# Performance work log

Hardware: AMD Instinct MI355X
Metric: run time of the kernel (lower is better)

The kernel has to match this reference:

```python
import jax, jax.numpy as jnp
import numpy as np
from jax import lax

# Dimensions (ModelArgs with d_model=1024)
B, L = 2, 1024
D_MODEL = 1024
D_INNER = 2048          # expand * d_model
D_STATE = 16
DT_RANK = 64            # ceil(d_model / 16)
D_CONV = 4


def setup_inputs() -> dict:
    key = jax.random.key(0)
    ks = jax.random.split(key, 8)
    sc = lambda k, shp, s: jax.random.normal(k, shp, dtype=jnp.float32) * s
    x = jax.random.normal(ks[0], (B, L, D_MODEL), dtype=jnp.float32)
    W_in = sc(ks[1], (2 * D_INNER, D_MODEL), 0.02)
    conv_w = sc(ks[2], (D_INNER, D_CONV), 0.2)
    conv_b = jnp.zeros((D_INNER,), jnp.float32)
    W_x = sc(ks[3], (DT_RANK + 2 * D_STATE, D_INNER), 0.02)
    dt_init_std = DT_RANK ** -0.5
    W_dt = jax.random.uniform(ks[4], (D_INNER, DT_RANK), jnp.float32,
                              -dt_init_std, dt_init_std)
    # dt_proj bias: inverse-softplus of dt ~ logUniform(dt_min, dt_max)
    dt_min, dt_max = 1e-3, 1e-1
    u = jax.random.uniform(ks[5], (D_INNER,), jnp.float32)
    dt = jnp.exp(u * (np.log(dt_max) - np.log(dt_min)) + np.log(dt_min))
    dt = jnp.clip(dt, 1e-4, None)
    b_dt = dt + jnp.log(-jnp.expm1(-dt))
    A_log = jnp.log(jnp.tile(jnp.arange(1, D_STATE + 1, dtype=jnp.float32)[None, :],
                             (D_INNER, 1)))
    D = jnp.ones((D_INNER,), jnp.float32)
    W_out = sc(ks[6], (D_MODEL, D_INNER), 0.02)
    return {"x": x, "W_in": W_in, "conv_w": conv_w, "conv_b": conv_b,
            "W_x": W_x, "W_dt": W_dt, "b_dt": b_dt, "A_log": A_log,
            "D": D, "W_out": W_out}


def reference(x, W_in, conv_w, conv_b, W_x, W_dt, b_dt, A_log, D, W_out):
    b, l, _ = x.shape
    d_in, n = A_log.shape
    k = conv_w.shape[1]

    # in_proj, split into conv branch and gating residual
    x_and_res = x @ W_in.T                                 # (b, l, 2*d_in)
    xz, res = jnp.split(x_and_res, [d_in], axis=-1)

    # Causal depthwise conv1d (kernel k, left-pad k-1, truncate to l)
    xp = jnp.pad(xz, ((0, 0), (k - 1, 0), (0, 0)))         # (b, l+k-1, d_in)
    xc = conv_b[None, None, :] + sum(
        xp[:, i:i + l, :] * conv_w[None, None, :, i] for i in range(k))
    xc = jax.nn.silu(xc)                                   # (b, l, d_in)

    # x_proj -> delta, B, C
    x_dbl = xc @ W_x.T                                     # (b, l, dt_rank+2n)
    dlt, Bm, Cm = jnp.split(x_dbl, [DT_RANK, DT_RANK + n], axis=-1)
    delta = jax.nn.softplus(dlt @ W_dt.T + b_dt)           # (b, l, d_in)

    # selective scan
    A = -jnp.exp(A_log)                                    # (d_in, n)
    dA = jnp.exp(delta[..., None] * A[None, None])         # (b, l, d_in, n)
    dBu = (delta * xc)[..., None] * Bm[:, :, None, :]      # (b, l, d_in, n)

    def step(h, inp):
        dA_t, dBu_t, C_t = inp                             # (b,d,n),(b,d,n),(b,n)
        h = dA_t * h + dBu_t
        y = jnp.einsum('bdn,bn->bd', h, C_t)
        return h, y

    h0 = jnp.zeros((b, d_in, n), xc.dtype)
    _, ys = lax.scan(step, h0, (dA.transpose(1, 0, 2, 3),
                                dBu.transpose(1, 0, 2, 3),
                                Cm.transpose(1, 0, 2)))
    y = ys.transpose(1, 0, 2) + xc * D[None, None, :]      # (b, l, d_in)

    y = y * jax.nn.silu(res)
    return y @ W_out.T                                     # (b, l, d_model)
```

## Files before the change

kernel.cpp:

```cpp
#include <hip/hip_runtime.h>
#include <hip/hip_bf16.h>
#include <cmath>

#define DEV __device__ __forceinline__

typedef float  f32x4  __attribute__((ext_vector_type(4)));
typedef __bf16 bf16x8 __attribute__((ext_vector_type(8)));
using u16 = unsigned short;

constexpr int CB   = 2;
constexpr int CLEN = 1024;
constexpr int CDM  = 1024;
constexpr int CDI  = 2048;
constexpr int CM   = CB * CLEN;
constexpr int NCHUNK = 32;
constexpr int CHL    = 32;
constexpr int LS     = 40;

DEV u16 f2bf(float f) {
  unsigned u = __builtin_bit_cast(unsigned, f);
  unsigned r = (u + 0x7fffu + ((u >> 16) & 1u)) >> 16;
  return (u16)r;
}
DEV float bf2f(u16 v) { return __builtin_bit_cast(float, ((unsigned)v) << 16); }

DEV ushort4 f4bf(float4 v) {
  ushort4 o;
  o.x = f2bf(v.x); o.y = f2bf(v.y); o.z = f2bf(v.z); o.w = f2bf(v.w);
  return o;
}

constexpr int CG_X   = 524288;
constexpr int CG_WIN = CG_X   + 1048576;
constexpr int CG_WDT = CG_WIN + 32768;
constexpr int CG_WO  = CG_WDT + 524288;
constexpr int CG_WX  = CG_WO  + 65536;

__global__ void cast_all_k(const float* __restrict__ x, const float* __restrict__ W_in,
                           const float* __restrict__ W_dt, const float* __restrict__ W_out,
                           const float* __restrict__ W_x,
                           u16* __restrict__ xb, u16* __restrict__ W_inb,
                           u16* __restrict__ W_dtb, u16* __restrict__ W_outb,
                           u16* __restrict__ W_xb)
{
  int i = blockIdx.x * blockDim.x + threadIdx.x;
  if (i < CG_X) {
    reinterpret_cast<ushort4*>(xb)[i] = f4bf(reinterpret_cast<const float4*>(x)[i]);
  } else if (i < CG_WIN) {
    int j = i - CG_X;
    reinterpret_cast<ushort4*>(W_inb)[j] = f4bf(reinterpret_cast<const float4*>(W_in)[j]);
  } else if (i < CG_WDT) {
    int j = i - CG_WIN;
    reinterpret_cast<ushort4*>(W_dtb)[j] = f4bf(reinterpret_cast<const float4*>(W_dt)[j]);
  } else if (i < CG_WO) {
    int j = i - CG_WDT;
    reinterpret_cast<ushort4*>(W_outb)[j] = f4bf(reinterpret_cast<const float4*>(W_out)[j]);
  } else {
    int j = i - CG_WO;
    int base = j * 4, row = base >> 11, col = base & 2047;
    float4 v = make_float4(0.f, 0.f, 0.f, 0.f);
    if (row < 96) v = *reinterpret_cast<const float4*>(W_x + row * 2048 + col);
    reinterpret_cast<ushort4*>(W_xb)[j] = f4bf(v);
  }
}

template <int EPI, int SPLITK>
__global__ __launch_bounds__(256, 2)
void gemm_bt(const u16* __restrict__ A, const u16* __restrict__ Bw,
             float* __restrict__ C, u16* __restrict__ Cb,
             const float* __restrict__ bias,
             int Nd, int Kd, int lda, int ldb, int ldc, size_t slice_stride)
{
  __shared__ u16 As[128 * LS];
  __shared__ u16 Bs[128 * LS];
  const int tid  = threadIdx.x;
  const int wave = tid >> 6;
  const int lane = tid & 63;
  const int wm = wave >> 1, wn = wave & 1;
  const int row0 = blockIdx.y * 128;
  const int col0 = blockIdx.x * 128;
  const int lr = lane >> 2;
  const int lc = (lane & 3) * 8;

  const int kper = Kd / SPLITK;
  const int kbeg = (SPLITK > 1) ? blockIdx.z * kper : 0;
  const int kend = kbeg + kper;
  float* Cz = (SPLITK > 1) ? C + (size_t)blockIdx.z * slice_stride : C;

  const u16* Ag = A  + (size_t)(row0 + wave * 16 + lr) * lda + lc;
  const u16* Bg = Bw + (size_t)(col0 + wave * 16 + lr) * ldb + lc;
  u16* Al0 = As + (wave * 16 + lr) * LS + lc;
  u16* Al1 = As + (64 + wave * 16 + lr) * LS + lc;
  u16* Bl0 = Bs + (wave * 16 + lr) * LS + lc;
  u16* Bl1 = Bs + (64 + wave * 16 + lr) * LS + lc;

  bf16x8 pa0 = *reinterpret_cast<const bf16x8*>(Ag + kbeg);
  bf16x8 pa1 = *reinterpret_cast<const bf16x8*>(Ag + (size_t)64 * lda + kbeg);
  bf16x8 pb0 = *reinterpret_cast<const bf16x8*>(Bg + kbeg);
  bf16x8 pb1 = *reinterpret_cast<const bf16x8*>(Bg + (size_t)64 * ldb + kbeg);

  f32x4 acc[4][4] = {};
  const int q  = lane >> 4;
  const int mr = lane & 15;

  for (int k0 = kbeg; k0 < kend; k0 += 32) {
    __syncthreads();
    *reinterpret_cast<bf16x8*>(Al0) = pa0;
    *reinterpret_cast<bf16x8*>(Al1) = pa1;
    *reinterpret_cast<bf16x8*>(Bl0) = pb0;
    *reinterpret_cast<bf16x8*>(Bl1) = pb1;
    __syncthreads();
    const int k1 = (k0 + 32 < kend) ? k0 + 32 : kbeg;
    pa0 = *reinterpret_cast<const bf16x8*>(Ag + k1);
    pa1 = *reinterpret_cast<const bf16x8*>(Ag + (size_t)64 * lda + k1);
    pb0 = *reinterpret_cast<const bf16x8*>(Bg + k1);
    pb1 = *reinterpret_cast<const bf16x8*>(Bg + (size_t)64 * ldb + k1);

    bf16x8 af[4], bfr[4];
#pragma unroll
    for (int t = 0; t < 4; ++t) {
      af[t]  = *reinterpret_cast<const bf16x8*>(As + (wm * 64 + t * 16 + mr) * LS + q * 8);
      bfr[t] = *reinterpret_cast<const bf16x8*>(Bs + (wn * 64 + t * 16 + mr) * LS + q * 8);
    }
#pragma unroll
    for (int mt = 0; mt < 4; ++mt)
#pragma unroll
      for (int nt = 0; nt < 4; ++nt)
        acc[mt][nt] = __builtin_amdgcn_mfma_f32_16x16x32_bf16(af[mt], bfr[nt], acc[mt][nt], 0, 0, 0);
  }

  const int cn = lane & 15;
#pragma unroll
  for (int mt = 0; mt < 4; ++mt)
#pragma unroll
    for (int nt = 0; nt < 4; ++nt)
#pragma unroll
      for (int r = 0; r < 4; ++r) {
        const int row = row0 + wm * 64 + mt * 16 + q * 4 + r;
        const int col = col0 + wn * 64 + nt * 16 + cn;
        float v = acc[mt][nt][r];
        if (EPI == 3) {
          v += bias[col];
          v = (v > 15.f) ? v : log1pf(__expf(v));
        }
        if (EPI == 0) Cz[(size_t)row * ldc + col] = v;
        else          Cb[(size_t)row * ldc + col] = f2bf(v);
      }
}

__global__ void xdbl_reduce_k(const float* __restrict__ part,
                              float* __restrict__ xdbl, u16* __restrict__ xdblb)
{
  int i = blockIdx.x * blockDim.x + threadIdx.x;
  float4 s = reinterpret_cast<const float4*>(part)[i];
#pragma unroll
  for (int z = 1; z < 16; ++z) {
    float4 p = reinterpret_cast<const float4*>(part + (size_t)z * CM * 128)[i];
    s.x += p.x; s.y += p.y; s.z += p.z; s.w += p.w;
  }
  reinterpret_cast<float4*>(xdbl)[i] = s;
  reinterpret_cast<ushort4*>(xdblb)[i] = f4bf(s);
}

__global__ void out_reduce_k(const float* __restrict__ part, float* __restrict__ out)
{
  int i = blockIdx.x * blockDim.x + threadIdx.x;
  float4 s = reinterpret_cast<const float4*>(part)[i];
#pragma unroll
  for (int z = 1; z < 4; ++z) {
    float4 p = reinterpret_cast<const float4*>(part + (size_t)z * CM * CDM)[i];
    s.x += p.x; s.y += p.y; s.z += p.z; s.w += p.w;
  }
  reinterpret_cast<float4*>(out)[i] = s;
}

__global__ void conv_silu_k(const u16* __restrict__ xzb, const float4* __restrict__ cw4,
                            const float* __restrict__ cb, u16* __restrict__ xcb)
{
  int idx = blockIdx.x * blockDim.x + threadIdx.x;
  int d8  = (idx & (CDI / 8 - 1)) * 8;
  int row = idx >> 8;
  int l   = row & (CLEN - 1);

  float4 wv[8];
#pragma unroll
  for (int j = 0; j < 8; ++j) wv[j] = cw4[d8 + j];
  float acc[8];
#pragma unroll
  for (int j = 0; j < 8; ++j) acc[j] = cb[d8 + j];

#pragma unroll
  for (int i = 0; i < 4; ++i) {
    int ls = l - 3 + i;
    if (ls >= 0) {
      bf16x8 v = *reinterpret_cast<const bf16x8*>(xzb + (size_t)(row - l + ls) * 4096 + d8);
#pragma unroll
      for (int j = 0; j < 8; ++j) {
        const float* wp = (const float*)&wv[j];
        acc[j] += (float)v[j] * wp[i];
      }
    }
  }
  bf16x8 o;
#pragma unroll
  for (int j = 0; j < 8; ++j) {
    float s = acc[j] / (1.f + __expf(-acc[j]));
    o[j] = (__bf16)s;
  }
  *reinterpret_cast<bf16x8*>(xcb + (size_t)row * CDI + d8) = o;
}

__global__ __launch_bounds__(256)
void scan_p1(const u16* __restrict__ delta_b, const u16* __restrict__ xcb,
             const float* __restrict__ xdbl, const float* __restrict__ A_log,
             float* __restrict__ P, float* __restrict__ S)
{
  __shared__ float sB[CHL * 16];
  const int t = threadIdx.x;
  const int d = blockIdx.x * 256 + t;
  const int c = blockIdx.y, b = blockIdx.z;

  for (int i = t; i < CHL * 16; i += 256) {
    int ll = i >> 4, n = i & 15;
    sB[i] = xdbl[(size_t)(b * CLEN + c * CHL + ll) * 128 + 64 + n];
  }
  __syncthreads();

  float An[16], Pv[16], Sv[16];
#pragma unroll
  for (int n = 0; n < 16; ++n) {
    An[n] = -__expf(A_log[d * 16 + n]);
    Pv[n] = 1.f; Sv[n] = 0.f;
  }
  const size_t rbase = (size_t)(b * CLEN + c * CHL) * CDI + d;
  for (int ll = 0; ll < CHL; ++ll) {
    float dl = bf2f(delta_b[rbase + (size_t)ll * CDI]);
    float u  = bf2f(xcb[rbase + (size_t)ll * CDI]);
    float du = dl * u;
#pragma unroll
    for (int n = 0; n < 16; ++n) {
      float a = __expf(dl * An[n]);
      Pv[n] *= a;
      Sv[n] = a * Sv[n] + du * sB[ll * 16 + n];
    }
  }
  const size_t o = (size_t)((b * NCHUNK + c) * 16) * CDI + d;
#pragma unroll
  for (int n = 0; n < 16; ++n) {
    P[o + (size_t)n * CDI] = Pv[n];
    S[o + (size_t)n * CDI] = Sv[n];
  }
}

__global__ void scan_p2(const float* __restrict__ P, const float* __restrict__ S,
                        float* __restrict__ Hin)
{
  const int t = threadIdx.x;
  const int d = blockIdx.x * 256 + t;
  const int n = blockIdx.y, b = blockIdx.z;
  float h = 0.f;
#pragma unroll 8
  for (int c = 0; c < NCHUNK; ++c) {
    size_t o = (size_t)((b * NCHUNK + c) * 16 + n) * CDI + d;
    Hin[o] = h;
    h = P[o] * h + S[o];
  }
}

__global__ __launch_bounds__(256)
void scan_p3(const u16* __restrict__ delta_b, const u16* __restrict__ xcb,
             const float* __restrict__ xdbl, const float* __restrict__ A_log,
             const float* __restrict__ Dvec, const u16* __restrict__ xzb,
             const float* __restrict__ Hin, u16* __restrict__ ybarb)
{
  __shared__ float sB[CHL * 16];
  __shared__ float sC[CHL * 16];
  const int t = threadIdx.x;
  const int d = blockIdx.x * 256 + t;
  const int c = blockIdx.y, b = blockIdx.z;

  for (int i = t; i < CHL * 16; i += 256) {
    int ll = i >> 4, n = i & 15;
    size_t ro = (size_t)(b * CLEN + c * CHL + ll) * 128;
    sB[i] = xdbl[ro + 64 + n];
    sC[i] = xdbl[ro + 80 + n];
  }
  __syncthreads();

  float An[16], h[16];
  const size_t ho = (size_t)((b * NCHUNK + c) * 16) * CDI + d;
#pragma unroll
  for (int n = 0; n < 16; ++n) {
    An[n] = -__expf(A_log[d * 16 + n]);
    h[n]  = Hin[ho + (size_t)n * CDI];
  }
  const float Dd = Dvec[d];
  const size_t rbase = (size_t)(b * CLEN + c * CHL);
  for (int ll = 0; ll < CHL; ++ll) {
    size_t e = (rbase + ll) * CDI + d;
    float dl = bf2f(delta_b[e]);
    float u  = bf2f(xcb[e]);
    float du = dl * u;
    float y  = 0.f;
#pragma unroll
    for (int n = 0; n < 16; ++n) {
      float a = __expf(dl * An[n]);
      h[n] = a * h[n] + du * sB[ll * 16 + n];
      y += h[n] * sC[ll * 16 + n];
    }
    y += u * Dd;
    float r = bf2f(xzb[(rbase + ll) * 4096 + CDI + d]);
    float sr = r / (1.f + __expf(-r));
    ybarb[e] = f2bf(y * sr);
  }
}

extern "C" void kernel_launch(void* const* d_in, const int* in_sizes, int n_in,
                              void* d_out, int out_size, void* d_ws, size_t ws_size,
                              hipStream_t stream)
{
  (void)in_sizes; (void)n_in; (void)out_size; (void)ws_size;
  const float* x      = (const float*)d_in[0];
  const float* W_in   = (const float*)d_in[1];
  const float* conv_w = (const float*)d_in[2];
  const float* conv_b = (const float*)d_in[3];
  const float* W_x    = (const float*)d_in[4];
  const float* W_dt   = (const float*)d_in[5];
  const float* b_dt   = (const float*)d_in[6];
  const float* A_log  = (const float*)d_in[7];
  const float* Dvec   = (const float*)d_in[8];
  const float* W_out  = (const float*)d_in[9];
  float* out = (float*)d_out;

  constexpr size_t MB = 1048576;
  char* w = (char*)d_ws;
  u16*   xzres_b = (u16*)(w + 0);
  u16*   xb      = (u16*)(w + 16 * MB);
  u16*   W_inb   = (u16*)(w + 20 * MB);
  u16*   xcb     = (u16*)(w + 28 * MB);
  u16*   delta_b = (u16*)(w + 36 * MB);
  float* xpart   = (float*)(w + 44 * MB);
  float* xdbl    = (float*)(w + 60 * MB);
  u16*   xdblb   = (u16*)(w + 61 * MB);
  u16*   W_xb    = (u16*)(w + 61 * MB + 512 * 1024);
  u16*   W_dtb   = (u16*)(w + 62 * MB);
  float* Pb      = (float*)(w + 63 * MB);
  float* Sb      = (float*)(w + 71 * MB);
  float* Hin     = (float*)(w + 79 * MB);
  u16*   ybarb   = (u16*)(w + 87 * MB);
  u16*   W_outb  = (u16*)(w + 95 * MB);
  float* opart   = (float*)(w + 99 * MB);

  dim3 blk(256);
  cast_all_k<<<CG_WX / 256, blk, 0, stream>>>(x, W_in, W_dt, W_out, W_x,
                                              xb, W_inb, W_dtb, W_outb, W_xb);
  gemm_bt<1, 1><<<dim3(32, 16), blk, 0, stream>>>(xb, W_inb, nullptr, xzres_b, nullptr,
                                                  4096, 1024, 1024, 1024, 4096, 0);
  conv_silu_k<<<(CB * CLEN * CDI / 8) / 256, blk, 0, stream>>>(
      xzres_b, (const float4*)conv_w, conv_b, xcb);
  gemm_bt<0, 16><<<dim3(1, 16, 16), blk, 0, stream>>>(xcb, W_xb, xpart, nullptr, nullptr,
                                                      128, 2048, 2048, 2048, 128,
                                                      (size_t)CM * 128);
  xdbl_reduce_k<<<(CM * 128 / 4) / 256, blk, 0, stream>>>(xpart, xdbl, xdblb);
  gemm_bt<3, 1><<<dim3(16, 16), blk, 0, stream>>>(xdblb, W_dtb, nullptr, delta_b, b_dt,
                                                  2048, 64, 128, 64, 2048, 0);
  scan_p1<<<dim3(8, NCHUNK, 2), blk, 0, stream>>>(delta_b, xcb, xdbl, A_log, Pb, Sb);
  scan_p2<<<dim3(8, 16, 2), blk, 0, stream>>>(Pb, Sb, Hin);
  scan_p3<<<dim3(8, NCHUNK, 2), blk, 0, stream>>>(delta_b, xcb, xdbl, A_log, Dvec,
                                                  xzres_b, Hin, ybarb);
  gemm_bt<0, 4><<<dim3(8, 16, 4), blk, 0, stream>>>(ybarb, W_outb, opart, nullptr, nullptr,
                                                    1024, 2048, 2048, 2048, 1024,
                                                    (size_t)CM * CDM);
  out_reduce_k<<<(CM * CDM / 4) / 256, blk, 0, stream>>>(opart, out);
}
```

Before: 259.1 us.

## Fuse three-pass chunked scan into single decoupled-lookback kernel

Replaces the three scan kernels (chunk-local pass, sequential carry pass, recompute-and-output pass) with one kernel. It uses atomic ticket ordering and per-chunk flags with decoupled lookback to pass inclusive states between chunks. Delta and x values are kept in registers between the local pass and the output pass, so they are not reloaded from global memory. This removes two launches and the separate P/S/Hin round trip. In exchange it adds spin-waiting on flags and serial dependence across chunk blocks, and register pressure rises from the 32-entry buffer.

Result: slower. 724.8 us (+179.8%).

```diff
diff --git a/kernel.cpp b/kernel.cpp
--- a/kernel.cpp
+++ b/kernel.cpp
@@ -41,9 +41,10 @@
                            const float* __restrict__ W_x,
                            u16* __restrict__ xb, u16* __restrict__ W_inb,
                            u16* __restrict__ W_dtb, u16* __restrict__ W_outb,
-                           u16* __restrict__ W_xb)
+                           u16* __restrict__ W_xb, int* __restrict__ flags)
 {
   int i = blockIdx.x * blockDim.x + threadIdx.x;
+  if (i < 1024) flags[i] = 0;
   if (i < CG_X) {
     reinterpret_cast<ushort4*>(xb)[i] = f4bf(reinterpret_cast<const float4*>(x)[i]);
   } else if (i < CG_WIN) {
@@ -210,74 +211,27 @@
   *reinterpret_cast<bf16x8*>(xcb + (size_t)row * CDI + d8) = o;
 }
 
-__global__ __launch_bounds__(256)
-void scan_p1(const u16* __restrict__ delta_b, const u16* __restrict__ xcb,
-             const float* __restrict__ xdbl, const float* __restrict__ A_log,
-             float* __restrict__ P, float* __restrict__ S)
-{
-  __shared__ float sB[CHL * 16];
-  const int t = threadIdx.x;
-  const int d = blockIdx.x * 256 + t;
-  const int c = blockIdx.y, b = blockIdx.z;
-
-  for (int i = t; i < CHL * 16; i += 256) {
-    int ll = i >> 4, n = i & 15;
-    sB[i] = xdbl[(size_t)(b * CLEN + c * CHL + ll) * 128 + 64 + n];
-  }
-  __syncthreads();
-
-  float An[16], Pv[16], Sv[16];
-#pragma unroll
-  for (int n = 0; n < 16; ++n) {
-    An[n] = -__expf(A_log[d * 16 + n]);
-    Pv[n] = 1.f; Sv[n] = 0.f;
-  }
-  const size_t rbase = (size_t)(b * CLEN + c * CHL) * CDI + d;
-  for (int ll = 0; ll < CHL; ++ll) {
-    float dl = bf2f(delta_b[rbase + (size_t)ll * CDI]);
-    float u  = bf2f(xcb[rbase + (size_t)ll * CDI]);
-    float du = dl * u;
-#pragma unroll
-    for (int n = 0; n < 16; ++n) {
-      float a = __expf(dl * An[n]);
-      Pv[n] *= a;
-      Sv[n] = a * Sv[n] + du * sB[ll * 16 + n];
-    }
-  }
-  const size_t o = (size_t)((b * NCHUNK + c) * 16) * CDI + d;
-#pragma unroll
-  for (int n = 0; n < 16; ++n) {
-    P[o + (size_t)n * CDI] = Pv[n];
-    S[o + (size_t)n * CDI] = Sv[n];
-  }
-}
-
-__global__ void scan_p2(const float* __restrict__ P, const float* __restrict__ S,
-                        float* __restrict__ Hin)
-{
-  const int t = threadIdx.x;
-  const int d = blockIdx.x * 256 + t;
-  const int n = blockIdx.y, b = blockIdx.z;
-  float h = 0.f;
-#pragma unroll 8
-  for (int c = 0; c < NCHUNK; ++c) {
-    size_t o = (size_t)((b * NCHUNK + c) * 16 + n) * CDI + d;
-    Hin[o] = h;
-    h = P[o] * h + S[o];
-  }
-}
-
-__global__ __launch_bounds__(256)
-void scan_p3(const u16* __restrict__ delta_b, const u16* __restrict__ xcb,
-             const float* __restrict__ xdbl, const float* __restrict__ A_log,
-             const float* __restrict__ Dvec, const u16* __restrict__ xzb,
-             const float* __restrict__ Hin, u16* __restrict__ ybarb)
+__global__ __launch_bounds__(256, 2)
+void scan_fused(const u16* __restrict__ delta_b, const u16* __restrict__ xcb,
+                const float* __restrict__ xdbl, const float* __restrict__ A_log,
+                const float* __restrict__ Dvec, const u16* __restrict__ xzb,
+                float* __restrict__ Ploc, float* __restrict__ Sloc,
+                float* __restrict__ Sinc, int* __restrict__ flags,
+                u16* __restrict__ ybarb)
 {
   __shared__ float sB[CHL * 16];
   __shared__ float sC[CHL * 16];
+  __shared__ int s_ticket;
   const int t = threadIdx.x;
-  const int d = blockIdx.x * 256 + t;
-  const int c = blockIdx.y, b = blockIdx.z;
+  if (t == 0) s_ticket = atomicAdd(&flags[512], 1);
+  __syncthreads();
+  const int ticket = s_ticket;
+  const int c    = ticket >> 4;
+  const int idx  = ticket & 15;
+  const int dblk = idx & 7;
+  const int b    = idx >> 3;
+  const int d    = dblk * 256 + t;
+  const int lane = t & 63;
 
   for (int i = t; i < CHL * 16; i += 256) {
     int ll = i >> 4, n = i & 15;
@@ -287,19 +241,96 @@
   }
   __syncthreads();
 
-  float An[16], h[16];
-  const size_t ho = (size_t)((b * NCHUNK + c) * 16) * CDI + d;
+  float An[16], Pv[16], Sv[16];
 #pragma unroll
   for (int n = 0; n < 16; ++n) {
     An[n] = -__expf(A_log[d * 16 + n]);
-    h[n]  = Hin[ho + (size_t)n * CDI];
-  }
+    Pv[n] = 1.f; Sv[n] = 0.f;
+  }
+
+  unsigned dx[CHL];
+  const size_t rbase = (size_t)(b * CLEN + c * CHL) * CDI + d;
+  for (int ll = 0; ll < CHL; ++ll) {
+    u16 dl16 = delta_b[rbase + (size_t)ll * CDI];
+    u16 uc16 = xcb[rbase + (size_t)ll * CDI];
+    dx[ll] = (unsigned)dl16 | ((unsigned)uc16 << 16);
+    float dl = bf2f(dl16), u = bf2f(uc16);
+    float du = dl * u;
+#pragma unroll
+    for (int n = 0; n < 16; ++n) {
+      float a = __expf(dl * An[n]);
+      Pv[n] *= a;
+      Sv[n] = a * Sv[n] + du * sB[ll * 16 + n];
+    }
+  }
+
+  const size_t pb = (size_t)((b * NCHUNK + c) * 16) * CDI + d;
+  const int myflag = (b * NCHUNK + c) * 8 + dblk;
+  float hin[16];
+  if (c == 0) {
+#pragma unroll
+    for (int n = 0; n < 16; ++n) { Sinc[pb + (size_t)n * CDI] = Sv[n]; hin[n] = 0.f; }
+    __threadfence(); __syncthreads();
+    if (t == 0) __hip_atomic_store(&flags[myflag], 2, __ATOMIC_RELEASE,
+                                   __HIP_MEMORY_SCOPE_AGENT);
+  } else {
+#pragma unroll
+    for (int n = 0; n < 16; ++n) {
+      Ploc[pb + (size_t)n * CDI] = Pv[n];
+      Sloc[pb + (size_t)n * CDI] = Sv[n];
+    }
+    __threadfence(); __syncthreads();
+    if (t == 0) __hip_atomic_store(&flags[myflag], 1, __ATOMIC_RELEASE,
+                                   __HIP_MEMORY_SCOPE_AGENT);
+    float accP[16], accS[16];
+#pragma unroll
+    for (int n = 0; n < 16; ++n) { accP[n] = 1.f; accS[n] = 0.f; }
+    int j = c - 1;
+    while (true) {
+      const int fj = (b * NCHUNK + j) * 8 + dblk;
+      int f = 0;
+      while (true) {
+        if (lane == 0)
+          f = __hip_atomic_load(&flags[fj], __ATOMIC_RELAXED, __HIP_MEMORY_SCOPE_AGENT);
+        f = __shfl(f, 0, 64);
+        if (f != 0) break;
+        __builtin_amdgcn_s_sleep(2);
+      }
+      __threadfence();
+      const size_t qb = (size_t)((b * NCHUNK + j) * 16) * CDI + d;
+      if (f == 2) {
+#pragma unroll
+        for (int n = 0; n < 16; ++n) {
+          float hj = Sinc[qb + (size_t)n * CDI];
+          hin[n] = accP[n] * hj + accS[n];
+        }
+        break;
+      } else {
+#pragma unroll
+        for (int n = 0; n < 16; ++n) {
+          float Pl = Ploc[qb + (size_t)n * CDI];
+          float Sl = Sloc[qb + (size_t)n * CDI];
+          accS[n] = accP[n] * Sl + accS[n];
+          accP[n] *= Pl;
+        }
+        --j;
+      }
+    }
+#pragma unroll
+    for (int n = 0; n < 16; ++n) Sinc[pb + (size_t)n * CDI] = Pv[n] * hin[n] + Sv[n];
+    __threadfence(); __syncthreads();
+    if (t == 0) __hip_atomic_store(&flags[myflag], 2, __ATOMIC_RELEASE,
+                                   __HIP_MEMORY_SCOPE_AGENT);
+  }
+
+  float h[16];
+#pragma unroll
+  for (int n = 0; n < 16; ++n) h[n] = hin[n];
   const float Dd = Dvec[d];
-  const size_t rbase = (size_t)(b * CLEN + c * CHL);
   for (int ll = 0; ll < CHL; ++ll) {
-    size_t e = (rbase + ll) * CDI + d;
-    float dl = bf2f(delta_b[e]);
-    float u  = bf2f(xcb[e]);
+    unsigned pv = dx[ll];
+    float dl = bf2f((u16)(pv & 0xffffu));
+    float u  = bf2f((u16)(pv >> 16));
     float du = dl * u;
     float y  = 0.f;
 #pragma unroll
@@ -309,9 +340,9 @@
       y += h[n] * sC[ll * 16 + n];
     }
     y += u * Dd;
-    float r = bf2f(xzb[(rbase + ll) * 4096 + CDI + d]);
+    float r = bf2f(xzb[(size_t)(b * CLEN + c * CHL + ll) * 4096 + CDI + d]);
     float sr = r / (1.f + __expf(-r));
-    ybarb[e] = f2bf(y * sr);
+    ybarb[rbase + (size_t)ll * CDI] = f2bf(y * sr);
   }
 }
 
@@ -344,16 +375,17 @@
   u16*   xdblb   = (u16*)(w + 61 * MB);
   u16*   W_xb    = (u16*)(w + 61 * MB + 512 * 1024);
   u16*   W_dtb   = (u16*)(w + 62 * MB);
-  float* Pb      = (float*)(w + 63 * MB);
-  float* Sb      = (float*)(w + 71 * MB);
-  float* Hin     = (float*)(w + 79 * MB);
+  int*   flags   = (int*)(w + 62 * MB + 256 * 1024);
+  float* Ploc    = (float*)(w + 63 * MB);
+  float* Sloc    = (float*)(w + 71 * MB);
+  float* Sinc    = (float*)(w + 79 * MB);
   u16*   ybarb   = (u16*)(w + 87 * MB);
   u16*   W_outb  = (u16*)(w + 95 * MB);
   float* opart   = (float*)(w + 99 * MB);
 
   dim3 blk(256);
   cast_all_k<<<CG_WX / 256, blk, 0, stream>>>(x, W_in, W_dt, W_out, W_x,
-                                              xb, W_inb, W_dtb, W_outb, W_xb);
+                                              xb, W_inb, W_dtb, W_outb, W_xb, flags);
   gemm_bt<1, 1><<<dim3(32, 16), blk, 0, stream>>>(xb, W_inb, nullptr, xzres_b, nullptr,
                                                   4096, 1024, 1024, 1024, 4096, 0);
   conv_silu_k<<<(CB * CLEN * CDI / 8) / 256, blk, 0, stream>>>(
@@ -364,10 +396,8 @@
   xdbl_reduce_k<<<(CM * 128 / 4) / 256, blk, 0, stream>>>(xpart, xdbl, xdblb);
   gemm_bt<3, 1><<<dim3(16, 16), blk, 0, stream>>>(xdblb, W_dtb, nullptr, delta_b, b_dt,
                                                   2048, 64, 128, 64, 2048, 0);
-  scan_p1<<<dim3(8, NCHUNK, 2), blk, 0, stream>>>(delta_b, xcb, xdbl, A_log, Pb, Sb);
-  scan_p2<<<dim3(8, 16, 2), blk, 0, stream>>>(Pb, Sb, Hin);
-  scan_p3<<<dim3(8, NCHUNK, 2), blk, 0, stream>>>(delta_b, xcb, xdbl, A_log, Dvec,
-                                                  xzres_b, Hin, ybarb);
+  scan_fused<<<dim3(512), blk, 0, stream>>>(delta_b, xcb, xdbl, A_log, Dvec,
+                                            xzres_b, Ploc, Sloc, Sinc, flags, ybarb);
   gemm_bt<0, 4><<<dim3(8, 16, 4), blk, 0, stream>>>(ybarb, W_outb, opart, nullptr, nullptr,
                                                     1024, 2048, 2048, 2048, 1024,
                                                     (size_t)CM * CDM);
```
